# Kernel tuning notes

Measured on AMD Instinct MI355X. Metric: run time of the kernel, lower is better.

## Reference

```python
import jax, jax.numpy as jnp
import numpy as np

DIM = 192
WIN = 7
HEADS = 6
SHIFT = 3
HID = 4 * DIM


def _ln(x, w, b, eps=1e-5):
    m = jnp.mean(x, axis=-1, keepdims=True)
    v = jnp.var(x, axis=-1, keepdims=True)
    return (x - m) * jax.lax.rsqrt(v + eps) * w + b


def setup_inputs() -> dict:
    key = jax.random.key(0)
    ks = jax.random.split(key, 8)
    B, C, H, W = 16, DIM, 56, 56
    s = lambda k, shape, fan: jax.random.normal(k, shape, jnp.float32) * (1.0 / np.sqrt(fan))
    return {
        "x": jax.random.normal(ks[0], (B, C, H, W), jnp.float32),
        "norm1_w": jnp.ones((C,), jnp.float32),
        "norm1_b": jnp.zeros((C,), jnp.float32),
        "qkv_w": s(ks[1], (3 * C, C), C),
        "qkv_b": jnp.zeros((3 * C,), jnp.float32),
        "proj_w": s(ks[2], (C, C), C),
        "proj_b": jnp.zeros((C,), jnp.float32),
        "norm2_w": jnp.ones((C,), jnp.float32),
        "norm2_b": jnp.zeros((C,), jnp.float32),
        "fc1_w": s(ks[3], (HID, C), C),
        "fc1_b": jnp.zeros((HID,), jnp.float32),
        "fc2_w": s(ks[4], (C, HID), HID),
        "fc2_b": jnp.zeros((C,), jnp.float32),
    }


def reference(x, norm1_w, norm1_b, qkv_w, qkv_b, proj_w, proj_b,
              norm2_w, norm2_b, fc1_w, fc1_b, fc2_w, fc2_b):
    B, C, H, W = x.shape
    shift = SHIFT if (H > WIN and W > WIN) else 0
    shortcut = x

    xl = jnp.transpose(x, (0, 2, 3, 1))            # B,H,W,C
    xl = _ln(xl, norm1_w, norm1_b)
    if shift > 0:
        xl = jnp.roll(xl, shift=(-shift, -shift), axis=(1, 2))
    nH, nW = H // WIN, W // WIN
    xw = xl.reshape(B, nH, WIN, nW, WIN, C)
    xw = jnp.transpose(xw, (0, 1, 3, 2, 4, 5)).reshape(-1, WIN * WIN, C)

    # window attention
    Bw, N, _ = xw.shape
    dh = C // HEADS
    qkv = jnp.einsum('bnc,oc->bno', xw, qkv_w) + qkv_b
    qkv = qkv.reshape(Bw, N, 3, HEADS, dh)
    q, k, v = qkv[:, :, 0], qkv[:, :, 1], qkv[:, :, 2]   # Bw,N,H,dh
    scale = dh ** -0.5
    attn = jnp.einsum('bnhd,bmhd->bhnm', q, k) * scale
    attn = jax.nn.softmax(attn, axis=-1)
    out = jnp.einsum('bhnm,bmhd->bnhd', attn, v).reshape(Bw, N, C)
    out = jnp.einsum('bnc,oc->bno', out, proj_w) + proj_b

    # window reverse -> B,H,W,C
    xl = out.reshape(B, nH, nW, WIN, WIN, C)
    xl = jnp.transpose(xl, (0, 1, 3, 2, 4, 5)).reshape(B, H, W, C)
    if shift > 0:
        xl = jnp.roll(xl, shift=(shift, shift), axis=(1, 2))

    # norm2 + MLP (note: original has NO attention residual)
    xl = _ln(xl, norm2_w, norm2_b)
    h = jnp.einsum('bhwc,oc->bhwo', xl, fc1_w) + fc1_b
    h = jax.nn.gelu(h, approximate=False)
    h = jnp.einsum('bhwo,co->bhwc', h, fc2_w) + fc2_b
    return jnp.transpose(h, (0, 3, 1, 2)) + shortcut
```

## Files before the change

kernel.cpp:

```cpp
#include <hip/hip_runtime.h>
#include <hip/hip_bf16.h>

typedef __bf16 bf16_t;
typedef __bf16 bf16x4 __attribute__((ext_vector_type(4)));
typedef __bf16 bf16x8 __attribute__((ext_vector_type(8)));
typedef float f32x4 __attribute__((ext_vector_type(4)));

#define MFMA16(a, b, c) __builtin_amdgcn_mfma_f32_16x16x32_bf16((a), (b), (c), 0, 0, 0)

__device__ __forceinline__ void gl16(const bf16_t* g, void* l) {
    __builtin_amdgcn_global_load_lds(
        (const __attribute__((address_space(1))) void*)g,
        (__attribute__((address_space(3))) void*)l, 16, 0, 0);
}

__device__ __forceinline__ float gelu_t(float u) {
    float t2 = fminf(u * (1.5957691216057308f + 0.07135481627f * u * u), 60.f);
    float e = __expf(t2);
    return u * e / (e + 1.f);
}


__global__ __launch_bounds__(256) void k_cvt(const float* __restrict__ qkvw,
                                             const float* __restrict__ projw,
                                             const float* __restrict__ fc1w,
                                             const float* __restrict__ fc2w,
                                             bf16_t* __restrict__ dst)
{
    int i = blockIdx.x * 256 + threadIdx.x;
    if (i >= 442368) return;
    float v;
    if (i < 110592)      v = qkvw[i];
    else if (i < 147456) v = projw[i - 110592];
    else if (i < 294912) v = fc1w[i - 147456];
    else                 v = fc2w[i - 294912];
    dst[i] = (bf16_t)v;
}

__global__ __launch_bounds__(1024) void k_ln1(const float* __restrict__ x,
                                              const float* __restrict__ gam,
                                              const float* __restrict__ bet,
                                              bf16_t* __restrict__ xw)
{
    __shared__ float tile[56][193];
    __shared__ bf16_t obuf[56 * 192];
    const int bh = blockIdx.x;
    const int b = bh / 56, h = bh % 56;
    const int tid = threadIdx.x;

    {
        const int g = tid >> 4, u = tid & 15;
        const float* xb = x + (long)b * 602112 + (long)h * 56;
        if (u < 14) {
            #pragma unroll
            for (int k = 0; k < 3; ++k) {
                const int c = g + 64 * k;
                float4 v = *(const float4*)(xb + (long)c * 3136 + u * 4);
                tile[u * 4 + 0][c] = v.x;
                tile[u * 4 + 1][c] = v.y;
                tile[u * 4 + 2][c] = v.z;
                tile[u * 4 + 3][c] = v.w;
            }
        }
    }
    __syncthreads();

    const int wave = tid >> 6, lane = tid & 63;
    const float g0 = gam[lane], g1 = gam[lane + 64], g2 = gam[lane + 128];
    const float b0 = bet[lane], b1 = bet[lane + 64], b2 = bet[lane + 128];
    for (int wp = wave; wp < 56; wp += 16) {
        float v0 = tile[wp][lane], v1 = tile[wp][lane + 64], v2 = tile[wp][lane + 128];
        float s = v0 + v1 + v2;
        float sq = v0 * v0 + v1 * v1 + v2 * v2;
        #pragma unroll
        for (int d = 1; d < 64; d <<= 1) { s += __shfl_xor(s, d); sq += __shfl_xor(sq, d); }
        float mean = s * (1.f / 192.f);
        float var  = sq * (1.f / 192.f) - mean * mean;
        float rs = rsqrtf(var + 1e-5f);
        const int wr = (wp + 53) % 56;
        bf16_t* o = obuf + wr * 192;
        o[lane]       = (bf16_t)((v0 - mean) * rs * g0 + b0);
        o[lane + 64]  = (bf16_t)((v1 - mean) * rs * g1 + b1);
        o[lane + 128] = (bf16_t)((v2 - mean) * rs * g2 + b2);
    }
    __syncthreads();

    const int hr = (h + 53) % 56;
    const int nh = hr / 7, ii = hr % 7;
    const long rband = ((long)b * 64 + (long)nh * 8) * 49 + (long)ii * 7;
    const int4* src = (const int4*)obuf;
    for (int q = tid; q < 1344; q += 1024) {
        const int g = q / 168, u = q % 168;
        const int jj = u / 24, ci = u % 24;
        const long r = rband + (long)g * 49 + jj;
        ((int4*)xw)[r * 24 + ci] = src[(g * 7 + jj) * 24 + ci];
    }
}

template<int EPI, int N>
__global__ __launch_bounds__(256) void k_gemm_1s(const bf16_t* __restrict__ A,
                                                 const bf16_t* __restrict__ W,
                                                 const float* __restrict__ bias,
                                                 bf16_t* __restrict__ outp)
{
    __shared__ bf16_t As[64 * 192];
    __shared__ bf16_t Bs[64 * 192];
    const int tid = threadIdx.x;
    const int wv = tid >> 6, ln = tid & 63;
    const int lrow = ln & 15, lkg = ln >> 4;
    const int r7 = lrow & 7;
    const int wm = (wv >> 1) * 32, wn = (wv & 1) * 32;
    const long m0 = (long)blockIdx.x * 64;
    const int n0 = blockIdx.y * 64;

    #pragma unroll
    for (int i = 0; i < 6; ++i) {
        const int off = ((wv * 6 + i) << 10) + ln * 16;
        const int row = off / 384;
        const int slot = (off % 384) >> 4;
        const int col = ((slot & 24) | ((slot & 7) ^ (row & 7))) << 3;
        gl16(A + (m0 + row) * 192 + col, (char*)As + ((wv * 6 + i) << 10));
    }
    #pragma unroll
    for (int i = 0; i < 6; ++i) {
        const int off = ((wv * 6 + i) << 10) + ln * 16;
        const int row = off / 384;
        const int slot = (off % 384) >> 4;
        const int col = ((slot & 24) | ((slot & 7) ^ (row & 7))) << 3;
        gl16(W + (long)(n0 + row) * 192 + col, (char*)Bs + ((wv * 6 + i) << 10));
    }
    __syncthreads();

    f32x4 acc[2][2];
    #pragma unroll
    for (int mi = 0; mi < 2; ++mi)
        #pragma unroll
        for (int ni = 0; ni < 2; ++ni)
            #pragma unroll
            for (int rg = 0; rg < 4; ++rg) acc[mi][ni][rg] = 0.f;

    #pragma unroll
    for (int kk = 0; kk < 6; ++kk) {
        const int s = kk * 4 + lkg;
        const int kb = ((s & 24) | ((s & 7) ^ r7)) << 4;
        bf16x8 af[2], bfr[2];
        #pragma unroll
        for (int mi = 0; mi < 2; ++mi)
            af[mi] = *(const bf16x8*)((const char*)As
                       + (wm + mi * 16 + lrow) * 384 + kb);
        #pragma unroll
        for (int ni = 0; ni < 2; ++ni)
            bfr[ni] = *(const bf16x8*)((const char*)Bs
                       + (wn + ni * 16 + lrow) * 384 + kb);
        #pragma unroll
        for (int mi = 0; mi < 2; ++mi)
            #pragma unroll
            for (int ni = 0; ni < 2; ++ni)
                acc[mi][ni] = MFMA16(bfr[ni], af[mi], acc[mi][ni]);
    }

    #pragma unroll
    for (int mi = 0; mi < 2; ++mi) {
        const long m = m0 + wm + mi * 16 + lrow;
        #pragma unroll
        for (int ni = 0; ni < 2; ++ni) {
            const int nb = n0 + wn + ni * 16 + lkg * 4;
            const float4 bv = *(const float4*)(bias + nb);
            float v[4] = { acc[mi][ni][0] + bv.x, acc[mi][ni][1] + bv.y,
                           acc[mi][ni][2] + bv.z, acc[mi][ni][3] + bv.w };
            bf16x4 o;
            #pragma unroll
            for (int rg = 0; rg < 4; ++rg) {
                float u = v[rg];
                if (EPI == 2) u = gelu_t(u);
                o[rg] = (bf16_t)u;
            }
            *(bf16x4*)(outp + m * N + nb) = o;
        }
    }
}

template<int EPI, int N, int K>
__global__ __launch_bounds__(256) void k_gemm(const bf16_t* __restrict__ A,
                                              const bf16_t* __restrict__ W,
                                              const float* __restrict__ bias,
                                              bf16_t* __restrict__ outp)
{
    __shared__ bf16_t As[128 * 64];
    __shared__ bf16_t Bs[64 * 64];
    const int tid = threadIdx.x;
    const int wv = tid >> 6, ln = tid & 63;
    const int lrow = ln & 15, lkg = ln >> 4;
    const int r7 = lrow & 7;
    const int wm = (wv >> 1) * 64, wn = (wv & 1) * 32;
    const long m0 = (long)blockIdx.x * 128;
    const int n0 = blockIdx.y * 64;

    f32x4 acc[4][2];
    #pragma unroll
    for (int mi = 0; mi < 4; ++mi)
        #pragma unroll
        for (int ni = 0; ni < 2; ++ni)
            #pragma unroll
            for (int rg = 0; rg < 4; ++rg) acc[mi][ni][rg] = 0.f;

    for (int t = 0; t < K / 64; ++t) {
        #pragma unroll
        for (int i = 0; i < 4; ++i) {
            const int off = ((wv * 4 + i) << 10) + ln * 16;
            const int row = off >> 7;
            const int c16 = ((off >> 4) & 7) ^ (row & 7);
            gl16(A + (m0 + row) * K + t * 64 + (c16 << 3),
                 (char*)As + ((wv * 4 + i) << 10));
        }
        #pragma unroll
        for (int i = 0; i < 2; ++i) {
            const int off = ((wv * 2 + i) << 10) + ln * 16;
            const int row = off >> 7;
            const int c16 = ((off >> 4) & 7) ^ (row & 7);
            gl16(W + (long)(n0 + row) * K + t * 64 + (c16 << 3),
                 (char*)Bs + ((wv * 2 + i) << 10));
        }
        __syncthreads();
        #pragma unroll
        for (int kk = 0; kk < 2; ++kk) {
            const int kb = (((kk << 2) | lkg) ^ r7) << 4;
            bf16x8 af[4], bfr[2];
            #pragma unroll
            for (int mi = 0; mi < 4; ++mi)
                af[mi] = *(const bf16x8*)((const char*)As
                           + (wm + mi * 16 + lrow) * 128 + kb);
            #pragma unroll
            for (int ni = 0; ni < 2; ++ni)
                bfr[ni] = *(const bf16x8*)((const char*)Bs
                           + (wn + ni * 16 + lrow) * 128 + kb);
            #pragma unroll
            for (int mi = 0; mi < 4; ++mi)
                #pragma unroll
                for (int ni = 0; ni < 2; ++ni)
                    acc[mi][ni] = MFMA16(bfr[ni], af[mi], acc[mi][ni]);
        }
        __syncthreads();
    }

    #pragma unroll
    for (int mi = 0; mi < 4; ++mi) {
        const long m = m0 + wm + mi * 16 + lrow;
        #pragma unroll
        for (int ni = 0; ni < 2; ++ni) {
            const int nb = n0 + wn + ni * 16 + lkg * 4;
            const float4 bv = *(const float4*)(bias + nb);
            float v[4] = { acc[mi][ni][0] + bv.x, acc[mi][ni][1] + bv.y,
                           acc[mi][ni][2] + bv.z, acc[mi][ni][3] + bv.w };
            bf16x4 o;
            #pragma unroll
            for (int rg = 0; rg < 4; ++rg) {
                float u = v[rg];
                if (EPI == 2) u = gelu_t(u);
                o[rg] = (bf16_t)u;
            }
            *(bf16x4*)(outp + m * N + nb) = o;
        }
    }
}

__global__ __launch_bounds__(256) void k_proj_ln(const bf16_t* __restrict__ A,
                                                 const bf16_t* __restrict__ W,
                                                 const float* __restrict__ bias,
                                                 const float* __restrict__ gam,
                                                 const float* __restrict__ bet,
                                                 bf16_t* __restrict__ out)
{
    __shared__ bf16_t As[64][72];
    __shared__ bf16_t Bs[192][72];
    const int tid = threadIdx.x;
    const int wave = tid >> 6, lane = tid & 63;
    const int lrow = lane & 15, lkg = lane >> 4;
    const int wm = wave * 16;
    const long m0 = (long)blockIdx.x * 64;

    f32x4 acc[12];
    #pragma unroll
    for (int ni = 0; ni < 12; ++ni)
        #pragma unroll
        for (int rg = 0; rg < 4; ++rg) acc[ni][rg] = 0.f;

    for (int k0 = 0; k0 < 192; k0 += 64) {
        #pragma unroll
        for (int it = 0; it < 2; ++it) {
            int e = (tid + it * 256) * 8;
            int r = e >> 6, c = e & 63;
            *(int4*)(&As[r][c]) = *(const int4*)(A + (m0 + r) * 192 + (k0 + c));
        }
        #pragma unroll
        for (int it = 0; it < 6; ++it) {
            int e = (tid + it * 256) * 8;
            int r = e >> 6, c = e & 63;
            *(int4*)(&Bs[r][c]) = *(const int4*)(W + (long)r * 192 + (k0 + c));
        }
        __syncthreads();
        #pragma unroll
        for (int kk = 0; kk < 64; kk += 32) {
            bf16x8 af = *(const bf16x8*)(&As[wm + lrow][kk + lkg * 8]);
            #pragma unroll
            for (int ni = 0; ni < 12; ++ni) {
                bf16x8 bfr = *(const bf16x8*)(&Bs[ni * 16 + lrow][kk + lkg * 8]);
                acc[ni] = MFMA16(af, bfr, acc[ni]);
            }
        }
        __syncthreads();
    }

    float bv[12];
    #pragma unroll
    for (int ni = 0; ni < 12; ++ni) bv[ni] = bias[ni * 16 + lrow];

    #pragma unroll
    for (int rg = 0; rg < 4; ++rg) {
        float val[12];
        float s = 0.f, sq = 0.f;
        #pragma unroll
        for (int ni = 0; ni < 12; ++ni) {
            val[ni] = acc[ni][rg] + bv[ni];
            s += val[ni];
            sq += val[ni] * val[ni];
        }
        #pragma unroll
        for (int d = 1; d < 16; d <<= 1) {
            s += __shfl_xor(s, d);
            sq += __shfl_xor(sq, d);
        }
        float mean = s * (1.f / 192.f);
        float var  = sq * (1.f / 192.f) - mean * mean;
        float rs = rsqrtf(var + 1e-5f);
        const long row = m0 + wm + lkg * 4 + rg;
        bf16_t* orow = out + row * 192;
        #pragma unroll
        for (int ni = 0; ni < 12; ++ni) {
            const int col = ni * 16 + lrow;
            orow[col] = (bf16_t)((val[ni] - mean) * rs * gam[col] + bet[col]);
        }
    }
}

__global__ __launch_bounds__(64) void k_attn(const bf16_t* __restrict__ qkv,
                                             bf16_t* __restrict__ aout)
{
    __shared__ bf16_t Pl[64][72];
    __shared__ bf16_t Vt[32][72];
    const int win = blockIdx.x, head = blockIdx.y;
    const int lane = threadIdx.x;
    const int lrow = lane & 15, lkg = lane >> 4;
    const bf16_t* base = qkv + (long)win * 28224 + head * 32;

    {
        const int m = lane;
        const int mc = (m < 49) ? m : 48;
        const int4* vr = (const int4*)(base + (long)mc * 576 + 384);
        #pragma unroll
        for (int c4 = 0; c4 < 4; ++c4) {
            int4 vv = vr[c4];
            if (m >= 49) vv = make_int4(0, 0, 0, 0);
            const bf16_t* pe = (const bf16_t*)&vv;
            #pragma unroll
            for (int e = 0; e < 8; ++e) Vt[c4 * 8 + e][m] = pe[e];
        }
    }

    bf16x8 z8;
    #pragma unroll
    for (int e = 0; e < 8; ++e) z8[e] = (bf16_t)0.f;
    bf16x8 qf[4], kf[4];
    #pragma unroll
    for (int t = 0; t < 4; ++t) {
        const int n = t * 16 + lrow;
        const int nc = (n < 49) ? n : 48;
        bf16x8 qv = *(const bf16x8*)(base + (long)nc * 576 + lkg * 8);
        bf16x8 kv = *(const bf16x8*)(base + (long)nc * 576 + 192 + lkg * 8);
        qf[t] = (n < 49) ? qv : z8;
        kf[t] = (n < 49) ? kv : z8;
    }
    f32x4 zf; zf[0] = zf[1] = zf[2] = zf[3] = 0.f;
    f32x4 S[4][4];
    #pragma unroll
    for (int mi = 0; mi < 4; ++mi)
        #pragma unroll
        for (int mj = 0; mj < 4; ++mj)
            S[mi][mj] = MFMA16(qf[mi], kf[mj], zf);

    const float scl = 0.17677669529663687f;
    #pragma unroll
    for (int mi = 0; mi < 4; ++mi) {
        #pragma unroll
        for (int rg = 0; rg < 4; ++rg) {
            float v0 = S[mi][0][rg] * scl;
            float v1 = S[mi][1][rg] * scl;
            float v2 = S[mi][2][rg] * scl;
            float v3 = (lrow == 0) ? S[mi][3][rg] * scl : -1e30f;
            float mx = fmaxf(fmaxf(v0, v1), fmaxf(v2, v3));
            #pragma unroll
            for (int d = 1; d < 16; d <<= 1) mx = fmaxf(mx, __shfl_xor(mx, d));
            float e0 = expf(v0 - mx), e1 = expf(v1 - mx), e2 = expf(v2 - mx);
            float e3 = (lrow == 0) ? expf(v3 - mx) : 0.f;
            float sm = e0 + e1 + e2 + e3;
            #pragma unroll
            for (int d = 1; d < 16; d <<= 1) sm += __shfl_xor(sm, d);
            float is = 1.f / sm;
            const int row = mi * 16 + lkg * 4 + rg;
            Pl[row][lrow]      = (bf16_t)(e0 * is);
            Pl[row][16 + lrow] = (bf16_t)(e1 * is);
            Pl[row][32 + lrow] = (bf16_t)(e2 * is);
            Pl[row][48 + lrow] = (bf16_t)(e3 * is);
        }
    }
    __syncthreads();

    f32x4 o[4][2];
    #pragma unroll
    for (int ni = 0; ni < 4; ++ni)
        #pragma unroll
        for (int di = 0; di < 2; ++di)
            #pragma unroll
            for (int rg = 0; rg < 4; ++rg) o[ni][di][rg] = 0.f;
    #pragma unroll
    for (int m0 = 0; m0 < 64; m0 += 32) {
        bf16x8 pf[4], vf[2];
        #pragma unroll
        for (int ni = 0; ni < 4; ++ni)
            pf[ni] = *(const bf16x8*)(&Pl[ni * 16 + lrow][m0 + lkg * 8]);
        #pragma unroll
        for (int di = 0; di < 2; ++di)
            vf[di] = *(const bf16x8*)(&Vt[di * 16 + lrow][m0 + lkg * 8]);
        #pragma unroll
        for (int ni = 0; ni < 4; ++ni)
            #pragma unroll
            for (int di = 0; di < 2; ++di)
                o[ni][di] = MFMA16(pf[ni], vf[di], o[ni][di]);
    }
    #pragma unroll
    for (int ni = 0; ni < 4; ++ni) {
        #pragma unroll
        for (int rg = 0; rg < 4; ++rg) {
            const int n = ni * 16 + lkg * 4 + rg;
            if (n < 49) {
                bf16_t* orow = aout + ((long)win * 49 + n) * 192 + head * 32;
                orow[lrow]      = (bf16_t)o[ni][0][rg];
                orow[16 + lrow] = (bf16_t)o[ni][1][rg];
            }
        }
    }
}

__global__ __launch_bounds__(1024) void k_final(const bf16_t* __restrict__ fb,
                                                const float* __restrict__ x,
                                                float* __restrict__ out)
{
    __shared__ float tile[56][199];
    const int bh = blockIdx.x;
    const int b = bh / 56, hq = bh % 56;
    const int tid = threadIdx.x;
    const int hr = (hq + 53) % 56;
    const int nh = hr / 7, ii = hr % 7;
    const long rband = ((long)b * 64 + (long)nh * 8) * 49 + (long)ii * 7;

    for (int q = tid; q < 1344; q += 1024) {
        const int g = q / 168, rem = q % 168;
        const int jj = rem / 24, ci = rem % 24;
        const long rr = rband + (long)g * 49 + jj;
        bf16x8 v = *(const bf16x8*)(fb + rr * 192 + ci * 8);
        const int wq = (g * 7 + jj + 3) % 56;
        #pragma unroll
        for (int e = 0; e < 8; ++e) tile[wq][ci * 8 + e] = (float)v[e];
    }
    __syncthreads();

    const int g = tid >> 4, u = tid & 15;
    if (u < 14) {
        #pragma unroll
        for (int k = 0; k < 3; ++k) {
            const int c = g + 64 * k;
            const long base = ((long)b * 192 + c) * 3136 + (long)hq * 56 + u * 4;
            float4 xv = *(const float4*)(x + base);
            float4 ov;
            ov.x = tile[u * 4 + 0][c] + xv.x;
            ov.y = tile[u * 4 + 1][c] + xv.y;
            ov.z = tile[u * 4 + 2][c] + xv.z;
            ov.w = tile[u * 4 + 3][c] + xv.w;
            *(float4*)(out + base) = ov;
        }
    }
}

extern "C" void kernel_launch(void* const* d_in, const int* in_sizes, int n_in,
                              void* d_out, int out_size, void* d_ws, size_t ws_size,
                              hipStream_t stream)
{
    const float* x     = (const float*)d_in[0];
    const float* n1w   = (const float*)d_in[1];
    const float* n1b   = (const float*)d_in[2];
    const float* qkvw  = (const float*)d_in[3];
    const float* qkvb  = (const float*)d_in[4];
    const float* projw = (const float*)d_in[5];
    const float* projb = (const float*)d_in[6];
    const float* n2w   = (const float*)d_in[7];
    const float* n2b   = (const float*)d_in[8];
    const float* fc1w  = (const float*)d_in[9];
    const float* fc1b  = (const float*)d_in[10];
    const float* fc2w  = (const float*)d_in[11];
    const float* fc2b  = (const float*)d_in[12];

    char* ws = (char*)d_ws;
    bf16_t* wqkv  = (bf16_t*)(ws);
    bf16_t* wproj = (bf16_t*)(ws + 221184);
    bf16_t* wfc1  = (bf16_t*)(ws + 294912);
    bf16_t* wfc2  = (bf16_t*)(ws + 589824);
    bf16_t* Xb    = (bf16_t*)(ws + 884736);
    bf16_t* QKV   = (bf16_t*)(ws + 20152320);
    bf16_t* Hb    = (bf16_t*)(ws + 77955072);
    bf16_t* H2    = (bf16_t*)(ws + 155025408);
    bf16_t* X2    = (bf16_t*)(ws + 174292992);

    k_cvt<<<1728, 256, 0, stream>>>(qkvw, projw, fc1w, fc2w, wqkv);
    k_ln1<<<896, 1024, 0, stream>>>(x, n1w, n1b, Xb);
    k_gemm_1s<0, 576><<<dim3(784, 9), 256, 0, stream>>>(Xb, wqkv, qkvb, QKV);
    k_attn<<<dim3(1024, 6), 64, 0, stream>>>(QKV, Xb);
    k_proj_ln<<<784, 256, 0, stream>>>(Xb, wproj, projb, n2w, n2b, X2);
    k_gemm_1s<2, 768><<<dim3(784, 12), 256, 0, stream>>>(X2, wfc1, fc1b, Hb);
    k_gemm<0, 192, 768><<<dim3(392, 3), 256, 0, stream>>>(Hb, wfc2, fc2b, H2);
    k_final<<<896, 1024, 0, stream>>>(H2, x, (float*)d_out);
}
```

Baseline: 210.1 us.

## Fuse fc1+GELU and fc2 into a single MLP kernel keeping hidden in LDS

Replaces the separate fc1 (with GELU) and fc2 GEMM launches with one kernel per 64-row tile. It computes 192-wide chunks of the hidden activation into shared memory and immediately accumulates them into the fc2 output. Weights are streamed through a small LDS buffer, with a register prefetch of the next 32-row slice. This removes the round trip of the large 768-wide hidden tensor through global memory and one launch. In exchange, weight loads are staged through registers with a sync every step, fewer blocks run, and the kernel uses more LDS.

```diff
diff --git a/kernel.cpp b/kernel.cpp
--- a/kernel.cpp
+++ b/kernel.cpp
@@ -180,86 +180,152 @@
     }
 }
 
-template<int EPI, int N, int K>
-__global__ __launch_bounds__(256) void k_gemm(const bf16_t* __restrict__ A,
-                                              const bf16_t* __restrict__ W,
-                                              const float* __restrict__ bias,
-                                              bf16_t* __restrict__ outp)
-{
-    __shared__ bf16_t As[128 * 64];
-    __shared__ bf16_t Bs[64 * 64];
+__global__ __launch_bounds__(256) void k_mlp(const bf16_t* __restrict__ A,
+                                             const bf16_t* __restrict__ W1,
+                                             const float* __restrict__ b1,
+                                             const bf16_t* __restrict__ W2,
+                                             const float* __restrict__ b2,
+                                             bf16_t* __restrict__ outp)
+{
+    __shared__ bf16_t Xs[64 * 192];
+    __shared__ bf16_t Hq[64 * 192];
+    __shared__ bf16_t Ws[32 * 192];
     const int tid = threadIdx.x;
     const int wv = tid >> 6, ln = tid & 63;
     const int lrow = ln & 15, lkg = ln >> 4;
-    const int r7 = lrow & 7;
-    const int wm = (wv >> 1) * 64, wn = (wv & 1) * 32;
-    const long m0 = (long)blockIdx.x * 128;
-    const int n0 = blockIdx.y * 64;
-
-    f32x4 acc[4][2];
-    #pragma unroll
-    for (int mi = 0; mi < 4; ++mi)
-        #pragma unroll
-        for (int ni = 0; ni < 2; ++ni)
-            #pragma unroll
-            for (int rg = 0; rg < 4; ++rg) acc[mi][ni][rg] = 0.f;
-
-    for (int t = 0; t < K / 64; ++t) {
-        #pragma unroll
-        for (int i = 0; i < 4; ++i) {
-            const int off = ((wv * 4 + i) << 10) + ln * 16;
-            const int row = off >> 7;
-            const int c16 = ((off >> 4) & 7) ^ (row & 7);
-            gl16(A + (m0 + row) * K + t * 64 + (c16 << 3),
-                 (char*)As + ((wv * 4 + i) << 10));
-        }
-        #pragma unroll
-        for (int i = 0; i < 2; ++i) {
-            const int off = ((wv * 2 + i) << 10) + ln * 16;
-            const int row = off >> 7;
-            const int c16 = ((off >> 4) & 7) ^ (row & 7);
-            gl16(W + (long)(n0 + row) * K + t * 64 + (c16 << 3),
-                 (char*)Bs + ((wv * 2 + i) << 10));
-        }
+    const long m0 = (long)blockIdx.x * 64;
+    const int wm = (wv >> 1) * 32;
+    const int wn16 = (wv & 1) * 16;
+    const int wn96 = (wv & 1) * 96;
+
+    #pragma unroll
+    for (int i = 0; i < 6; ++i) {
+        const int off = ((wv * 6 + i) << 10) + ln * 16;
+        const int row = off / 384;
+        const int slot = (off % 384) >> 4;
+        const int col = ((slot & 24) | ((slot & 7) ^ (row & 7))) << 3;
+        gl16(A + (m0 + row) * 192 + col, (char*)Xs + ((wv * 6 + i) << 10));
+    }
+
+    int ldsoff[3]; long w1off[3], w2off[3];
+    #pragma unroll
+    for (int i = 0; i < 3; ++i) {
+        const int off = ((wv * 3 + i) << 10) + ln * 16;
+        ldsoff[i] = off;
+        const int ra1 = off / 384, sa1 = (off % 384) >> 4;
+        w1off[i] = (long)ra1 * 192 + (((sa1 & 24) | ((sa1 & 7) ^ (ra1 & 7))) << 3);
+        const int ra2 = off >> 6, sa2 = (off >> 4) & 3;
+        w2off[i] = (long)ra2 * 768 + ((sa2 ^ (ra2 & 3)) << 3);
+    }
+
+    int4 ra, rb, rc;
+    auto issue = [&](int qn, int rn) {
+        if (rn < 6) {
+            const bf16_t* b = W1 + (long)(qn * 192 + rn * 32) * 192;
+            ra = *(const int4*)(b + w1off[0]);
+            rb = *(const int4*)(b + w1off[1]);
+            rc = *(const int4*)(b + w1off[2]);
+        } else {
+            const bf16_t* b = W2 + qn * 192 + (rn - 6) * 32;
+            ra = *(const int4*)(b + w2off[0]);
+            rb = *(const int4*)(b + w2off[1]);
+            rc = *(const int4*)(b + w2off[2]);
+        }
+    };
+
+    f32x4 acc2[2][6];
+    #pragma unroll
+    for (int mi = 0; mi < 2; ++mi)
+        #pragma unroll
+        for (int ni = 0; ni < 6; ++ni)
+            #pragma unroll
+            for (int rg = 0; rg < 4; ++rg) acc2[mi][ni][rg] = 0.f;
+
+    issue(0, 0);
+    __syncthreads();
+
+    int q = 0, r = 0;
+    #pragma unroll 1
+    for (int p = 0; p < 48; ++p) {
+        *(int4*)((char*)Ws + ldsoff[0]) = ra;
+        *(int4*)((char*)Ws + ldsoff[1]) = rb;
+        *(int4*)((char*)Ws + ldsoff[2]) = rc;
         __syncthreads();
-        #pragma unroll
-        for (int kk = 0; kk < 2; ++kk) {
-            const int kb = (((kk << 2) | lkg) ^ r7) << 4;
-            bf16x8 af[4], bfr[2];
-            #pragma unroll
-            for (int mi = 0; mi < 4; ++mi)
-                af[mi] = *(const bf16x8*)((const char*)As
-                           + (wm + mi * 16 + lrow) * 128 + kb);
-            #pragma unroll
-            for (int ni = 0; ni < 2; ++ni)
-                bfr[ni] = *(const bf16x8*)((const char*)Bs
-                           + (wn + ni * 16 + lrow) * 128 + kb);
-            #pragma unroll
-            for (int mi = 0; mi < 4; ++mi)
+        int qn = q, rn = r + 1;
+        if (rn == 12) { rn = 0; qn = q + 1; }
+        if (p + 1 < 48) issue(qn, rn);
+
+        if (r < 6) {
+            f32x4 acc1[2];
+            #pragma unroll
+            for (int mi = 0; mi < 2; ++mi)
                 #pragma unroll
-                for (int ni = 0; ni < 2; ++ni)
-                    acc[mi][ni] = MFMA16(bfr[ni], af[mi], acc[mi][ni]);
+                for (int rg = 0; rg < 4; ++rg) acc1[mi][rg] = 0.f;
+            #pragma unroll
+            for (int kk = 0; kk < 6; ++kk) {
+                const int sb = kk * 4 + lkg;
+                const int rowb = wn16 + lrow;
+                bf16x8 bfr = *(const bf16x8*)((const char*)Ws + rowb * 384
+                               + (((sb & 24) | ((sb & 7) ^ (rowb & 7))) << 4));
+                #pragma unroll
+                for (int mi = 0; mi < 2; ++mi) {
+                    const int rowa = wm + mi * 16 + lrow;
+                    bf16x8 af = *(const bf16x8*)((const char*)Xs + rowa * 384
+                                  + (((sb & 24) | ((sb & 7) ^ (rowa & 7))) << 4));
+                    acc1[mi] = MFMA16(bfr, af, acc1[mi]);
+                }
+            }
+            const int qcol = r * 32 + wn16 + lkg * 4;
+            const float4 bv = *(const float4*)(b1 + q * 192 + qcol);
+            const int slot = qcol >> 3;
+            #pragma unroll
+            for (int mi = 0; mi < 2; ++mi) {
+                const int rowm = wm + mi * 16 + lrow;
+                bf16x4 o;
+                o[0] = (bf16_t)gelu_t(acc1[mi][0] + bv.x);
+                o[1] = (bf16_t)gelu_t(acc1[mi][1] + bv.y);
+                o[2] = (bf16_t)gelu_t(acc1[mi][2] + bv.z);
+                o[3] = (bf16_t)gelu_t(acc1[mi][3] + bv.w);
+                *(bf16x4*)((char*)Hq + rowm * 384
+                    + (((slot & 24) | ((slot & 7) ^ (rowm & 7))) << 4)
+                    + ((qcol & 7) << 1)) = o;
+            }
+        } else {
+            const int sh = (r - 6) * 4 + lkg;
+            bf16x8 af[2];
+            #pragma unroll
+            for (int mi = 0; mi < 2; ++mi) {
+                const int rowa = wm + mi * 16 + lrow;
+                af[mi] = *(const bf16x8*)((const char*)Hq + rowa * 384
+                           + (((sh & 24) | ((sh & 7) ^ (rowa & 7))) << 4));
+            }
+            #pragma unroll
+            for (int ni = 0; ni < 6; ++ni) {
+                const int rowb = wn96 + ni * 16 + lrow;
+                bf16x8 bfr = *(const bf16x8*)((const char*)Ws + rowb * 64
+                               + ((lkg ^ (rowb & 3)) << 4));
+                #pragma unroll
+                for (int mi = 0; mi < 2; ++mi)
+                    acc2[mi][ni] = MFMA16(bfr, af[mi], acc2[mi][ni]);
+            }
         }
         __syncthreads();
-    }
-
-    #pragma unroll
-    for (int mi = 0; mi < 4; ++mi) {
+        q = qn; r = rn;
+    }
+
+    #pragma unroll
+    for (int mi = 0; mi < 2; ++mi) {
         const long m = m0 + wm + mi * 16 + lrow;
         #pragma unroll
-        for (int ni = 0; ni < 2; ++ni) {
-            const int nb = n0 + wn + ni * 16 + lkg * 4;
-            const float4 bv = *(const float4*)(bias + nb);
-            float v[4] = { acc[mi][ni][0] + bv.x, acc[mi][ni][1] + bv.y,
-                           acc[mi][ni][2] + bv.z, acc[mi][ni][3] + bv.w };
+        for (int ni = 0; ni < 6; ++ni) {
+            const int nb = wn96 + ni * 16 + lkg * 4;
+            const float4 bv = *(const float4*)(b2 + nb);
             bf16x4 o;
-            #pragma unroll
-            for (int rg = 0; rg < 4; ++rg) {
-                float u = v[rg];
-                if (EPI == 2) u = gelu_t(u);
-                o[rg] = (bf16_t)u;
-            }
-            *(bf16x4*)(outp + m * N + nb) = o;
+            o[0] = (bf16_t)(acc2[mi][ni][0] + bv.x);
+            o[1] = (bf16_t)(acc2[mi][ni][1] + bv.y);
+            o[2] = (bf16_t)(acc2[mi][ni][2] + bv.z);
+            o[3] = (bf16_t)(acc2[mi][ni][3] + bv.w);
+            *(bf16x4*)(outp + m * 192 + nb) = o;
         }
     }
 }
@@ -516,7 +582,6 @@
     bf16_t* wfc2  = (bf16_t*)(ws + 589824);
     bf16_t* Xb    = (bf16_t*)(ws + 884736);
     bf16_t* QKV   = (bf16_t*)(ws + 20152320);
-    bf16_t* Hb    = (bf16_t*)(ws + 77955072);
     bf16_t* H2    = (bf16_t*)(ws + 155025408);
     bf16_t* X2    = (bf16_t*)(ws + 174292992);
 
@@ -525,7 +590,6 @@
     k_gemm_1s<0, 576><<<dim3(784, 9), 256, 0, stream>>>(Xb, wqkv, qkvb, QKV);
     k_attn<<<dim3(1024, 6), 64, 0, stream>>>(QKV, Xb);
     k_proj_ln<<<784, 256, 0, stream>>>(Xb, wproj, projb, n2w, n2b, X2);
-    k_gemm_1s<2, 768><<<dim3(784, 12), 256, 0, stream>>>(X2, wfc1, fc1b, Hb);
-    k_gemm<0, 192, 768><<<dim3(392, 3), 256, 0, stream>>>(Hb, wfc2, fc2b, H2);
+    k_mlp<<<784, 256, 0, stream>>>(X2, wfc1, fc1b, wfc2, fc2b, H2);
     k_final<<<896, 1024, 0, stream>>>(H2, x, (float*)d_out);
 }
```

New measurement: 228.3 us. 8.7% more time.
